# Performance work log

Measured on AMD Instinct MI355X. Metric: run time of the kernel, lower is better.

The kernel has to match this reference:

```python
import jax, jax.numpy as jnp
import numpy as np
import math

B, T, C, H = 4, 2048, 1024, 16
D = C // H  # head dim = 64


def setup_inputs() -> dict:
    key = jax.random.key(0)
    ks = jax.random.split(key, 5)
    scale = 0.02
    x = jax.random.normal(ks[0], (B, T, C), dtype=jnp.float32)
    # torch nn.Linear(n_embd, 3*n_embd): weight [3C, C]; we store transposed [C, 3C]
    W_kqv = jax.random.normal(ks[1], (C, 3 * C), dtype=jnp.float32) * scale
    b_kqv = jnp.zeros((3 * C,), dtype=jnp.float32)
    W_proj = jax.random.normal(ks[2], (C, C), dtype=jnp.float32) * scale
    b_proj = jnp.zeros((C,), dtype=jnp.float32)
    padding_mask = jnp.ones((B, T), dtype=jnp.int32)  # 1 = valid token
    return {"x": x, "W_kqv": W_kqv, "b_kqv": b_kqv, "W_proj": W_proj,
            "b_proj": b_proj, "padding_mask": padding_mask}


def reference(x, W_kqv, b_kqv, W_proj, b_proj, padding_mask):
    Bx, Tx, Cx = x.shape
    kqv = x @ W_kqv + b_kqv                      # [B,T,3C]
    # original splits as k, q, v (in that order)
    k, q, v = jnp.split(kqv, 3, axis=2)
    def heads(t):
        return t.reshape(Bx, Tx, H, D).transpose(0, 2, 1, 3)  # [B,H,T,D]
    k, q, v = heads(k), heads(q), heads(v)
    att = jnp.einsum('bhqd,bhkd->bhqk', q, k) * (1.0 / math.sqrt(D))  # [B,H,T,T]
    causal = jnp.tril(jnp.ones((Tx, Tx), dtype=bool))[None, None]     # [1,1,T,T]
    valid = causal & (padding_mask[:, None, None, :] != 0)            # [B,1,T,T] broadcast
    neg_inf = jnp.finfo(att.dtype).min
    att = jnp.where(valid, att, neg_inf)
    att = jax.nn.softmax(att, axis=-1)
    y = jnp.einsum('bhqk,bhkd->bhqd', att, v)    # [B,H,T,D]
    y = y.transpose(0, 2, 1, 3).reshape(Bx, Tx, Cx)
    return y @ W_proj + b_proj
```

## Files before the change

### kernel.cpp

```cpp
#include <hip/hip_runtime.h>


typedef short bf16x8 __attribute__((ext_vector_type(8)));
typedef float floatx4 __attribute__((ext_vector_type(4)));

#define MFMA16(a, b, c) __builtin_amdgcn_mfma_f32_16x16x32_bf16(a, b, c, 0, 0, 0)

#define ASYNC_COPY16(gp, lp)                                                   \
  __builtin_amdgcn_global_load_lds(                                            \
      (__attribute__((address_space(1))) void*)(gp),                           \
      (__attribute__((address_space(3))) void*)(lp), 16, 0, 0)

#define DRAIN_VMCNT() asm volatile("s_waitcnt vmcnt(0)" ::: "memory")
#define WAIT_VMCNT6() asm volatile("s_waitcnt vmcnt(6)" ::: "memory")

#if defined(__has_builtin)
#if __has_builtin(__builtin_amdgcn_exp2f)
#define EXP2(x) __builtin_amdgcn_exp2f(x)
#endif
#endif
#ifndef EXP2
#define EXP2(x) exp2f(x)
#endif

__device__ __forceinline__ short f2bf(float f) {
  union { float f; unsigned u; } c;
  c.f = f;
  unsigned r = c.u + 0x7fffu + ((c.u >> 16) & 1u);
  return (short)(r >> 16);
}

__global__ __launch_bounds__(256) void prep(const float* __restrict__ x,
                                            short* __restrict__ xb,
                                            const float* __restrict__ Wkqv,
                                            short* __restrict__ Wkqvt,
                                            const float* __restrict__ Wproj,
                                            short* __restrict__ Wprojt) {
  __shared__ float buf[64][65];
  const int t = threadIdx.x;
  const int bx = blockIdx.x;
  if (bx < 8192) {
    int i = (bx * 256 + t) * 4;
    float4 v = *(const float4*)&x[i];
    short4 o;
    o.x = f2bf(v.x); o.y = f2bf(v.y); o.z = f2bf(v.z); o.w = f2bf(v.w);
    *(short4*)&xb[i] = o;
    return;
  }
  const int tb = bx - 8192;
  const int nb = tb & 63, kb = tb >> 6;
  const float* in;
  short* out;
  int N, n0;
  if (nb < 48) { in = Wkqv; out = Wkqvt; N = 3072; n0 = nb * 64; }
  else         { in = Wproj; out = Wprojt; N = 1024; n0 = (nb - 48) * 64; }
  const int k0 = kb * 64;
#pragma unroll
  for (int i = 0; i < 4; ++i) {
    int s = t + i * 256;
    int row = s >> 4, c4 = (s & 15) * 4;
    float4 v = *(const float4*)&in[(size_t)(k0 + row) * N + n0 + c4];
    buf[row][c4] = v.x; buf[row][c4 + 1] = v.y;
    buf[row][c4 + 2] = v.z; buf[row][c4 + 3] = v.w;
  }
  __syncthreads();
#pragma unroll
  for (int i = 0; i < 2; ++i) {
    int u = t + i * 256;
    int rn = u >> 3, ch = (u & 7) * 8;
    short tmp[8];
#pragma unroll
    for (int j = 0; j < 8; ++j) tmp[j] = f2bf(buf[ch + j][rn]);
    *(uint4*)&out[(size_t)(n0 + rn) * 1024 + k0 + ch] = *(uint4*)tmp;
  }
}

template <int MODE>
__global__ __launch_bounds__(512, 2) void gemm_ph256(const short* __restrict__ A,
                                                     const short* __restrict__ Bt,
                                                     const float* __restrict__ bias,
                                                     void* __restrict__ Cout,
                                                     int M, int N, int K) {
  __shared__ short smem[73728];
  const int tid = threadIdx.x;
  const int lane = tid & 63;
  const int wv = tid >> 6;
  const int l15 = lane & 15, quad = lane >> 4;
  const int xr = l15 & 7;
  const int m0 = blockIdx.y * 128, n0 = blockIdx.x * 256;
  const int wm = (wv >> 2) * 64, wn = (wv & 3) * 64;
  const int NT = K >> 6;

  floatx4 acc[4][4] = {};

#define STAGE_A(kt, bs, j)                                                     \
  { int c_ = (j) * 512 + tid;                                                  \
    int r_ = c_ >> 3, ch_ = (c_ & 7) ^ (r_ & 7);                               \
    ASYNC_COPY16(&A[(size_t)(m0 + r_) * K + (kt) * 64 + ch_ * 8],              \
                 &smem[(bs) * 8192 + c_ * 8]); }
#define STAGE_B(kt, bs, j)                                                     \
  { int c_ = (j) * 512 + tid;                                                  \
    int r_ = c_ >> 3, ch_ = (c_ & 7) ^ (r_ & 7);                               \
    ASYNC_COPY16(&Bt[(size_t)(n0 + r_) * K + (kt) * 64 + ch_ * 8],             \
                 &smem[24576 + (bs) * 16384 + c_ * 8]); }

  STAGE_A(0, 0, 0); STAGE_A(0, 0, 1);
  STAGE_B(0, 0, 0); STAGE_B(0, 0, 1); STAGE_B(0, 0, 2); STAGE_B(0, 0, 3);
  STAGE_A(1, 1, 0); STAGE_A(1, 1, 1);
  STAGE_B(1, 1, 0); STAGE_B(1, 1, 1); STAGE_B(1, 1, 2); STAGE_B(1, 1, 3);
  WAIT_VMCNT6();
  __builtin_amdgcn_s_barrier();

  int cur = 0, nxt = 2;
  for (int kt = 0; kt < NT; ++kt) {
    const bool st = (kt + 2 < NT);
    const short* Asr = &smem[cur * 8192];
    const short* Bsr = &smem[24576 + cur * 16384];

    if (st) { STAGE_A(kt + 2, nxt, 0); STAGE_A(kt + 2, nxt, 1); STAGE_B(kt + 2, nxt, 0); }
    bf16x8 af[4][2], bf0[2][2];
#pragma unroll
    for (int mi = 0; mi < 4; ++mi)
#pragma unroll
      for (int s = 0; s < 2; ++s)
        af[mi][s] = *(const bf16x8*)
            &Asr[(wm + mi * 16 + l15) * 64 + (((s * 4 + quad) ^ xr) * 8)];
#pragma unroll
    for (int nj = 0; nj < 2; ++nj)
#pragma unroll
      for (int s = 0; s < 2; ++s)
        bf0[nj][s] = *(const bf16x8*)
            &Bsr[(wn + nj * 16 + l15) * 64 + (((s * 4 + quad) ^ xr) * 8)];
    __builtin_amdgcn_s_setprio(1);
#pragma unroll
    for (int s = 0; s < 2; ++s)
#pragma unroll
      for (int mi = 0; mi < 4; ++mi)
#pragma unroll
        for (int nj = 0; nj < 2; ++nj)
          acc[mi][nj] = MFMA16(af[mi][s], bf0[nj][s], acc[mi][nj]);
    __builtin_amdgcn_s_setprio(0);
    __builtin_amdgcn_s_barrier();

    if (st) { STAGE_B(kt + 2, nxt, 1); STAGE_B(kt + 2, nxt, 2); STAGE_B(kt + 2, nxt, 3); }
    bf16x8 bf1[2][2];
#pragma unroll
    for (int nj = 0; nj < 2; ++nj)
#pragma unroll
      for (int s = 0; s < 2; ++s)
        bf1[nj][s] = *(const bf16x8*)
            &Bsr[(wn + (2 + nj) * 16 + l15) * 64 + (((s * 4 + quad) ^ xr) * 8)];
    __builtin_amdgcn_s_setprio(1);
#pragma unroll
    for (int s = 0; s < 2; ++s)
#pragma unroll
      for (int mi = 0; mi < 4; ++mi)
#pragma unroll
        for (int nj = 0; nj < 2; ++nj)
          acc[mi][2 + nj] = MFMA16(af[mi][s], bf1[nj][s], acc[mi][2 + nj]);
    __builtin_amdgcn_s_setprio(0);
    if (st) { WAIT_VMCNT6(); } else { DRAIN_VMCNT(); }
    __builtin_amdgcn_s_barrier();
    cur = (cur == 2) ? 0 : cur + 1;
    nxt = (nxt == 2) ? 0 : nxt + 1;
  }
#undef STAGE_A
#undef STAGE_B

  if (MODE == 0) {
    float* outf = (float*)Cout;
#pragma unroll
    for (int ni = 0; ni < 4; ++ni) {
      int col = n0 + wn + ni * 16 + l15;
      float bv = bias[col];
#pragma unroll
      for (int mi = 0; mi < 4; ++mi) {
#pragma unroll
        for (int rr = 0; rr < 4; ++rr) {
          int row = m0 + wm + mi * 16 + quad * 4 + rr;
          outf[(size_t)row * N + col] = acc[mi][ni][rr] + bv;
        }
      }
    }
  } else {
    short* outs = (short*)Cout;
    const size_t QOFF = (size_t)64 * 2048 * 64;
    const int sec = n0 >> 10;
    short* Es = smem;
    if (sec < 2) {
#pragma unroll
      for (int ni = 0; ni < 4; ++ni) {
        int c = wn + ni * 16 + l15;
        float bv = bias[n0 + c];
#pragma unroll
        for (int mi = 0; mi < 4; ++mi) {
          int r0 = wm + mi * 16 + quad * 4;
#pragma unroll
          for (int rr = 0; rr < 4; ++rr) {
            int r = r0 + rr;
            Es[r * 256 + (c ^ (((r >> 2) & 3) << 4))] = f2bf(acc[mi][ni][rr] + bv);
          }
        }
      }
    } else {
#pragma unroll
      for (int ni = 0; ni < 4; ++ni) {
        int c = wn + ni * 16 + l15;
        float bv = bias[n0 + c];
#pragma unroll
        for (int mi = 0; mi < 4; ++mi) {
          int r0 = wm + mi * 16 + quad * 4;
#pragma unroll
          for (int rr = 0; rr < 4; ++rr) {
            int r = r0 + rr;
            Es[c * 128 + (r ^ ((c & 7) << 3))] = f2bf(acc[mi][ni][rr] + bv);
          }
        }
      }
    }
    __syncthreads();
    if (sec < 2) {
#pragma unroll
      for (int jj = 0; jj < 8; ++jj) {
        int idx = jj * 512 + tid;
        int rr2 = idx >> 5;
        int cc2 = (idx & 31) * 8;
        uint4 v = *(const uint4*)&Es[rr2 * 256 + (cc2 ^ (((rr2 >> 2) & 3) << 4))];
        int colg = n0 + cc2;
        int hh = (colg >> 6) & 15, dd = colg & 63;
        int row = m0 + rr2, bb = row >> 11, tt = row & 2047;
        *(uint4*)(outs + (size_t)sec * QOFF +
                  (((size_t)(bb * 16 + hh) * 2048 + tt) * 64 + dd)) = v;
      }
    } else {
#pragma unroll
      for (int jj = 0; jj < 8; ++jj) {
        int idx = jj * 512 + tid;
        int cd = idx >> 4;
        int rb = (idx & 15) * 8;
        uint4 v = *(const uint4*)&Es[cd * 128 + (rb ^ ((cd & 7) << 3))];
        int colg = n0 + cd;
        int hh = (colg >> 6) & 15, dd = colg & 63;
        int trow = m0 + rb, bb = trow >> 11, tt = trow & 2047;
        *(uint4*)(outs + 2 * QOFF +
                  ((size_t)(bb * 16 + hh) * 64 + dd) * 2048 + tt) = v;
      }
    }
  }
}

__global__ __launch_bounds__(256, 3) void attn_flash8(const short* __restrict__ Qd,
                                                      const short* __restrict__ Kd,
                                                      const short* __restrict__ Vd,
                                                      const int* __restrict__ pmask,
                                                      short* __restrict__ y) {
  constexpr int T = 2048, C = 1024;
  __shared__ short Ks[2][64 * 64];
  __shared__ short Vs[2][64 * 64];
  __shared__ short Ps[4][32][64];

  const int tid = threadIdx.x;
  const int lane = tid & 63, w = tid >> 6;
  const int l15 = lane & 15, quad = lane >> 4;
  const int xr = l15 & 7;
  const int lin = blockIdx.x;
  const int qb = 15 - (lin >> 6);
  const int bh = lin & 63;
  const int b = bh >> 4, h = bh & 15;
  const short* Qb = Qd + (size_t)bh * T * 64;
  const short* Kb = Kd + (size_t)bh * T * 64;
  const short* Vb = Vd + (size_t)bh * 64 * T;
  const int* pmi = &pmask[b * T];
  const int q0 = qb * 128;
  const int nt = (q0 >> 6) + 2;

  const float SCALE2 = 0.18033688011112042f;

#define STAGE_KV(t, buf)                                                       \
  {                                                                            \
    const short* ksrc_ = Kb + (size_t)((t) * 64) * 64;                         \
    const short* vsrc_ = Vb + (t) * 64;                                        \
    _Pragma("unroll")                                                          \
    for (int j_ = 0; j_ < 2; ++j_) {                                           \
      int c_ = j_ * 256 + tid;                                                 \
      int r_ = c_ >> 3, cc_ = (c_ & 7) ^ (r_ & 7);                             \
      ASYNC_COPY16(ksrc_ + r_ * 64 + cc_ * 8, &Ks[buf][c_ * 8]);               \
      ASYNC_COPY16(vsrc_ + (size_t)r_ * T + cc_ * 8, &Vs[buf][c_ * 8]);        \
    }                                                                          \
  }

  bf16x8 qf[2][2];
#pragma unroll
  for (int mi = 0; mi < 2; ++mi) {
    const short* qp = Qb + (size_t)(q0 + w * 32 + mi * 16 + l15) * 64;
    qf[mi][0] = *(const bf16x8*)&qp[quad * 8];
    qf[mi][1] = *(const bf16x8*)&qp[32 + quad * 8];
  }

  floatx4 Oacc[2][4] = {};
  float lpart[2] = {};

  STAGE_KV(0, 0);
  DRAIN_VMCNT();
  __syncthreads();

  int cur = 0;
#pragma unroll 1
  for (int t = 0; t < nt; ++t) {
    const int k0 = t * 64;
    if (t + 1 < nt) STAGE_KV(t + 1, cur ^ 1);

    floatx4 Sacc[2][4] = {};
#pragma unroll
    for (int s = 0; s < 2; ++s) {
#pragma unroll
      for (int n4 = 0; n4 < 4; ++n4) {
        bf16x8 bK = *(const bf16x8*)
            &Ks[cur][(n4 * 16 + l15) * 64 + (((s * 4 + quad) ^ xr) * 8)];
        Sacc[0][n4] = MFMA16(bK, qf[0][s], Sacc[0][n4]);
        Sacc[1][n4] = MFMA16(bK, qf[1][s], Sacc[1][n4]);
      }
    }

    if (k0 < q0) {
#pragma unroll
      for (int n4 = 0; n4 < 4; ++n4) {
        int4 pm4 = *(const int4*)&pmi[k0 + n4 * 16 + quad * 4];
        float pb[4];
        pb[0] = pm4.x ? 0.0f : -3.0e38f;
        pb[1] = pm4.y ? 0.0f : -3.0e38f;
        pb[2] = pm4.z ? 0.0f : -3.0e38f;
        pb[3] = pm4.w ? 0.0f : -3.0e38f;
#pragma unroll
        for (int mi = 0; mi < 2; ++mi) {
          float p[4];
#pragma unroll
          for (int rr = 0; rr < 4; ++rr) {
            p[rr] = EXP2(fmaf(Sacc[mi][n4][rr], SCALE2, pb[rr]));
            lpart[mi] += p[rr];
          }
          unsigned lo, hi;
          asm("v_cvt_pk_bf16_f32 %0, %1, %2" : "=v"(lo) : "v"(p[0]), "v"(p[1]));
          asm("v_cvt_pk_bf16_f32 %0, %1, %2" : "=v"(hi) : "v"(p[2]), "v"(p[3]));
          uint2 pk; pk.x = lo; pk.y = hi;
          *(uint2*)&Ps[w][mi * 16 + l15]
                      [((n4 * 2 + (quad >> 1)) ^ xr) * 8 + (quad & 1) * 4] = pk;
        }
      }
    } else {
#pragma unroll
      for (int n4 = 0; n4 < 4; ++n4) {
        int4 pm4 = *(const int4*)&pmi[k0 + n4 * 16 + quad * 4];
        float pb[4];
        pb[0] = pm4.x ? 0.0f : -3.0e38f;
        pb[1] = pm4.y ? 0.0f : -3.0e38f;
        pb[2] = pm4.z ? 0.0f : -3.0e38f;
        pb[3] = pm4.w ? 0.0f : -3.0e38f;
        const int colb = n4 * 16 + quad * 4;
#pragma unroll
        for (int mi = 0; mi < 2; ++mi) {
          const int rowb = (q0 - k0) + w * 32 + mi * 16 + l15;
          float p[4];
#pragma unroll
          for (int rr = 0; rr < 4; ++rr) {
            float v = EXP2(fmaf(Sacc[mi][n4][rr], SCALE2, pb[rr]));
            if (colb + rr > rowb) v = 0.f;
            p[rr] = v;
            lpart[mi] += v;
          }
          unsigned lo, hi;
          asm("v_cvt_pk_bf16_f32 %0, %1, %2" : "=v"(lo) : "v"(p[0]), "v"(p[1]));
          asm("v_cvt_pk_bf16_f32 %0, %1, %2" : "=v"(hi) : "v"(p[2]), "v"(p[3]));
          uint2 pk; pk.x = lo; pk.y = hi;
          *(uint2*)&Ps[w][mi * 16 + l15]
                      [((n4 * 2 + (quad >> 1)) ^ xr) * 8 + (quad & 1) * 4] = pk;
        }
      }
    }

#pragma unroll
    for (int ks2 = 0; ks2 < 2; ++ks2) {
      const int pco = (((ks2 * 4 + quad) ^ xr) * 8);
      bf16x8 ap0 = *(const bf16x8*)&Ps[w][l15][pco];
      bf16x8 ap1 = *(const bf16x8*)&Ps[w][16 + l15][pco];
#pragma unroll
      for (int nd = 0; nd < 4; ++nd) {
        bf16x8 bV = *(const bf16x8*)
            &Vs[cur][(nd * 16 + l15) * 64 + (((ks2 * 4 + quad) ^ xr) * 8)];
        Oacc[0][nd] = MFMA16(ap0, bV, Oacc[0][nd]);
        Oacc[1][nd] = MFMA16(ap1, bV, Oacc[1][nd]);
      }
    }

    DRAIN_VMCNT();
    __syncthreads();
    cur ^= 1;
  }
#undef STAGE_KV

#pragma unroll
  for (int mi = 0; mi < 2; ++mi) {
    float s = lpart[mi];
    s += __shfl_xor(s, 16, 64);
    s += __shfl_xor(s, 32, 64);
    float inv_l[4];
#pragma unroll
    for (int rr = 0; rr < 4; ++rr)
      inv_l[rr] = 1.0f / __shfl(s, quad * 4 + rr, 16);
#pragma unroll
    for (int n = 0; n < 4; ++n) {
      int dcol = n * 16 + l15;
#pragma unroll
      for (int rr = 0; rr < 4; ++rr) {
        int rowq = q0 + w * 32 + mi * 16 + quad * 4 + rr;
        y[((size_t)(b * T + rowq)) * C + h * 64 + dcol] =
            f2bf(Oacc[mi][n][rr] * inv_l[rr]);
      }
    }
  }
}

extern "C" void kernel_launch(void* const* d_in, const int* in_sizes, int n_in,
                              void* d_out, int out_size, void* d_ws, size_t ws_size,
                              hipStream_t stream) {
  constexpr int B = 4, T = 2048, C = 1024;
  constexpr int M = B * T;
  constexpr int N1 = 3 * C;

  const float* x      = (const float*)d_in[0];
  const float* W_kqv  = (const float*)d_in[1];
  const float* b_kqv  = (const float*)d_in[2];
  const float* W_proj = (const float*)d_in[3];
  const float* b_proj = (const float*)d_in[4];
  const int*   pmask  = (const int*)d_in[5];
  float* out = (float*)d_out;

  const size_t QOFF = (size_t)64 * T * 64;

  short* xb     = (short*)d_ws;
  short* Wkqvt  = xb + (size_t)M * C;
  short* Wprojt = Wkqvt + (size_t)N1 * C;
  short* qkv    = Wprojt + (size_t)C * C;
  short* yb     = xb;

  short* Kd = qkv;
  short* Qd = qkv + QOFF;
  short* Vd = qkv + 2 * QOFF;

  prep<<<dim3(8192 + 1024), 256, 0, stream>>>(x, xb, W_kqv, Wkqvt, W_proj, Wprojt);

  gemm_ph256<2><<<dim3(N1 / 256, M / 128), 512, 0, stream>>>(xb, Wkqvt, b_kqv, Kd, M, N1, C);

  attn_flash8<<<dim3(1024), 256, 0, stream>>>(Qd, Kd, Vd, pmask, yb);

  gemm_ph256<0><<<dim3(C / 256, M / 128), 512, 0, stream>>>(yb, Wprojt, b_proj, out, M, C, C);
}
```

Measured before the change: 252.3 us.

## Add 128x128 double-buffered projection GEMM and remap workgroups for L2 locality

```diff
diff --git a/kernel.cpp b/kernel.cpp
--- a/kernel.cpp
+++ b/kernel.cpp
@@ -87,7 +87,11 @@
   const int wv = tid >> 6;
   const int l15 = lane & 15, quad = lane >> 4;
   const int xr = l15 & 7;
-  const int m0 = blockIdx.y * 128, n0 = blockIdx.x * 256;
+  int lin = blockIdx.y * gridDim.x + blockIdx.x;
+  const int nwg = gridDim.x * gridDim.y;
+  lin = (lin & 7) * (nwg >> 3) + (lin >> 3);
+  const int bx = lin % gridDim.x, by = lin / gridDim.x;
+  const int m0 = by * 128, n0 = bx * 256;
   const int wm = (wv >> 2) * 64, wn = (wv & 3) * 64;
   const int NT = K >> 6;
 
@@ -167,22 +171,7 @@
 #undef STAGE_A
 #undef STAGE_B
 
-  if (MODE == 0) {
-    float* outf = (float*)Cout;
-#pragma unroll
-    for (int ni = 0; ni < 4; ++ni) {
-      int col = n0 + wn + ni * 16 + l15;
-      float bv = bias[col];
-#pragma unroll
-      for (int mi = 0; mi < 4; ++mi) {
-#pragma unroll
-        for (int rr = 0; rr < 4; ++rr) {
-          int row = m0 + wm + mi * 16 + quad * 4 + rr;
-          outf[(size_t)row * N + col] = acc[mi][ni][rr] + bv;
-        }
-      }
-    }
-  } else {
+  {
     short* outs = (short*)Cout;
     const size_t QOFF = (size_t)64 * 2048 * 64;
     const int sec = n0 >> 10;
@@ -244,6 +233,82 @@
         int trow = m0 + rb, bb = trow >> 11, tt = trow & 2047;
         *(uint4*)(outs + 2 * QOFF +
                   ((size_t)(bb * 16 + hh) * 64 + dd) * 2048 + tt) = v;
+      }
+    }
+  }
+}
+
+__global__ __launch_bounds__(256, 2) void gemm_dbuf128(const short* __restrict__ A,
+                                                       const short* __restrict__ Bt,
+                                                       const float* __restrict__ bias,
+                                                       float* __restrict__ outf,
+                                                       int M, int N, int K) {
+  __shared__ short As[2][8192];
+  __shared__ short Bs[2][8192];
+  const int tid = threadIdx.x;
+  const int lane = tid & 63;
+  const int wv = tid >> 6;
+  const int l15 = lane & 15, quad = lane >> 4;
+  const int xr = l15 & 7;
+  int lin = blockIdx.y * gridDim.x + blockIdx.x;
+  const int nwg = gridDim.x * gridDim.y;
+  lin = (lin & 7) * (nwg >> 3) + (lin >> 3);
+  const int bx = lin & (gridDim.x - 1), by = lin / gridDim.x;
+  const int m0 = by * 128, n0 = bx * 128;
+  const int wm = (wv >> 1) * 64, wn = (wv & 1) * 64;
+  const int NT = K >> 6;
+
+  floatx4 acc[4][4] = {};
+
+#define STAGE_AB(kt, bs)                                                       \
+  { _Pragma("unroll")                                                          \
+    for (int j_ = 0; j_ < 4; ++j_) {                                           \
+      int c_ = j_ * 256 + tid;                                                 \
+      int r_ = c_ >> 3, ch_ = (c_ & 7) ^ (r_ & 7);                             \
+      ASYNC_COPY16(&A[(size_t)(m0 + r_) * K + (kt) * 64 + ch_ * 8],            \
+                   &As[bs][c_ * 8]);                                           \
+      ASYNC_COPY16(&Bt[(size_t)(n0 + r_) * K + (kt) * 64 + ch_ * 8],           \
+                   &Bs[bs][c_ * 8]);                                           \
+    } }
+
+  STAGE_AB(0, 0);
+  DRAIN_VMCNT();
+  __syncthreads();
+
+  int cur = 0;
+  for (int kt = 0; kt < NT; ++kt) {
+    if (kt + 1 < NT) STAGE_AB(kt + 1, cur ^ 1);
+#pragma unroll
+    for (int s = 0; s < 2; ++s) {
+      const int chs = ((s * 4 + quad) ^ xr) * 8;
+      bf16x8 af[4], bfr[4];
+#pragma unroll
+      for (int i = 0; i < 4; ++i) {
+        af[i]  = *(const bf16x8*)&As[cur][(wm + i * 16 + l15) * 64 + chs];
+        bfr[i] = *(const bf16x8*)&Bs[cur][(wn + i * 16 + l15) * 64 + chs];
+      }
+#pragma unroll
+      for (int mi = 0; mi < 4; ++mi)
+#pragma unroll
+        for (int ni = 0; ni < 4; ++ni)
+          acc[mi][ni] = MFMA16(af[mi], bfr[ni], acc[mi][ni]);
+    }
+    DRAIN_VMCNT();
+    __syncthreads();
+    cur ^= 1;
+  }
+#undef STAGE_AB
+
+#pragma unroll
+  for (int ni = 0; ni < 4; ++ni) {
+    int col = n0 + wn + ni * 16 + l15;
+    float bv = bias[col];
+#pragma unroll
+    for (int mi = 0; mi < 4; ++mi) {
+#pragma unroll
+      for (int rr = 0; rr < 4; ++rr) {
+        int row = m0 + wm + mi * 16 + quad * 4 + rr;
+        outf[(size_t)row * N + col] = acc[mi][ni][rr] + bv;
       }
     }
   }
@@ -453,5 +518,5 @@
 
   attn_flash8<<<dim3(1024), 256, 0, stream>>>(Qd, Kd, Vd, pmask, yb);
 
-  gemm_ph256<0><<<dim3(C / 256, M / 128), 512, 0, stream>>>(yb, Wprojt, b_proj, out, M, C, C);
+  gemm_dbuf128<<<dim3(C / 128, M / 128), 256, 0, stream>>>(yb, Wprojt, b_proj, out, M, C, C);
 }
```

Result: no change. 248.1 us (-1.7%).
